# Optimization experiments

Hardware: AMD Instinct MI355X
Metric: run time of the kernel (lower is better)

The kernel has to match this reference:

```python
import jax, jax.numpy as jnp
import numpy as np

DIM = 96
HEADS = 6
WS = 8                      # window_size
OWS = int(WS * 0.5) + WS    # overlap_win_size = 12
PAD = (OWS - WS) // 2       # 2
Dd = Hh = Ww = 24
B = 1
L = Dd * Hh * Ww
MLP_H = DIM * 2
TBL = (WS + OWS - 1) ** 3   # 6859 relative-position-bias entries


def setup_inputs() -> dict:
    key = jax.random.key(0)
    ks = jax.random.split(key, 8)
    def n(k, shape, s=0.02):
        return jax.random.normal(k, shape, jnp.float32) * s
    return {
        "x": jax.random.normal(ks[0], (B, L, DIM), jnp.float32),
        "ln1_w": jnp.ones((DIM,), jnp.float32),
        "ln1_b": jnp.zeros((DIM,), jnp.float32),
        "qkv_w": n(ks[1], (3 * DIM, DIM)),
        "qkv_b": jnp.zeros((3 * DIM,), jnp.float32),
        "rpb": n(ks[2], (TBL, HEADS)),
        "proj_w": n(ks[3], (DIM, DIM)),
        "proj_b": jnp.zeros((DIM,), jnp.float32),
        "ln2_w": jnp.ones((DIM,), jnp.float32),
        "ln2_b": jnp.zeros((DIM,), jnp.float32),
        "fc1_w": n(ks[4], (MLP_H, DIM)),
        "fc1_b": jnp.zeros((MLP_H,), jnp.float32),
        "fc2_w": n(ks[5], (DIM, MLP_H)),
        "fc2_b": jnp.zeros((DIM,), jnp.float32),
        "rpi": jax.random.randint(ks[6], (WS ** 3, OWS ** 3), 0, TBL),
        "D": Dd, "H": Hh, "W": Ww,
    }


def _ln(x, w, b):
    m = jnp.mean(x, -1, keepdims=True)
    v = jnp.var(x, -1, keepdims=True)
    return (x - m) / jnp.sqrt(v + 1e-5) * w + b


def _ocab3d(x, ln1_w, ln1_b, qkv_w, qkv_b, rpb, proj_w, proj_b,
            ln2_w, ln2_b, fc1_w, fc1_b, fc2_w, fc2_b, rpi, D, H, W):
    Bz, Lz, C = x.shape
    hd = C // HEADS
    scale = hd ** -0.5
    shortcut = x

    xn = _ln(x, ln1_w, ln1_b).reshape(Bz, D, H, W, C)
    qkv = xn @ qkv_w.T + qkv_b                   # [B,D,H,W,3C]
    q = qkv[..., :C]
    kv = qkv[..., C:]                            # cat(k, v) on channels, [B,D,H,W,2C]

    nD, nH, nW = D // WS, H // WS, W // WS
    nw = nD * nH * nW

    # non-overlapping query windows -> [B*nw, WS^3, C]
    qw = q.reshape(Bz, nD, WS, nH, WS, nW, WS, C)
    qw = qw.transpose(0, 1, 3, 5, 2, 4, 6, 7).reshape(Bz * nw, WS ** 3, C)

    # overlapping kv windows via pad + strided gather (mirrors F.pad + unfold)
    kvp = jnp.pad(kv, ((0, 0), (PAD, PAD), (PAD, PAD), (PAD, PAD), (0, 0)))
    idx_d = (jnp.arange(nD) * WS)[:, None] + jnp.arange(OWS)[None, :]
    idx_h = (jnp.arange(nH) * WS)[:, None] + jnp.arange(OWS)[None, :]
    idx_w = (jnp.arange(nW) * WS)[:, None] + jnp.arange(OWS)[None, :]
    kw = kvp[:, idx_d]                 # [B,nD,OWS,Hp,Wp,2C]
    kw = kw[:, :, :, idx_h]            # [B,nD,OWS,nH,OWS,Wp,2C]
    kw = kw[:, :, :, :, :, idx_w]      # [B,nD,OWS,nH,OWS,nW,OWS,2C]
    kw = kw.transpose(0, 1, 3, 5, 2, 4, 6, 7).reshape(Bz * nw, OWS ** 3, 2 * C)
    kk, vv = kw[..., :C], kw[..., C:]

    qh = qw.reshape(-1, WS ** 3, HEADS, hd).transpose(0, 2, 1, 3) * scale
    kh = kk.reshape(-1, OWS ** 3, HEADS, hd).transpose(0, 2, 1, 3)
    vh = vv.reshape(-1, OWS ** 3, HEADS, hd).transpose(0, 2, 1, 3)

    attn = jnp.einsum('bhqd,bhkd->bhqk', qh, kh)               # [B*nw,H,512,1728]
    bias = rpb[rpi.reshape(-1)].reshape(WS ** 3, OWS ** 3, HEADS).transpose(2, 0, 1)
    attn = jax.nn.softmax(attn + bias[None], axis=-1)
    out = jnp.einsum('bhqk,bhkd->bhqd', attn, vh)
    out = out.transpose(0, 2, 1, 3).reshape(Bz * nw, WS ** 3, C)

    # window reverse -> [B, L, C]
    out = out.reshape(Bz, nD, nH, nW, WS, WS, WS, C)
    out = out.transpose(0, 1, 4, 2, 5, 3, 6, 7).reshape(Bz, D * H * W, C)

    x2 = out @ proj_w.T + proj_b + shortcut
    h1 = jax.nn.gelu(_ln(x2, ln2_w, ln2_b) @ fc1_w.T + fc1_b, approximate=False)
    return x2 + (h1 @ fc2_w.T + fc2_b)


def reference(x, ln1_w, ln1_b, qkv_w, qkv_b, rpb, proj_w, proj_b,
              ln2_w, ln2_b, fc1_w, fc1_b, fc2_w, fc2_b, rpi, D, H, W):
    return _ocab3d(x, ln1_w, ln1_b, qkv_w, qkv_b, rpb, proj_w, proj_b,
                   ln2_w, ln2_b, fc1_w, fc1_b, fc2_w, fc2_b, rpi, D, H, W)
```

## Files before the change

kernel.cpp:

```cpp
#include <hip/hip_runtime.h>
#include <math.h>

#define DIMC   96
#define NHEADS 6
#define HD     16
#define WSZ    8
#define OWSZ   12
#define PADW   2
#define DD     24
#define LTOK   13824
#define NWIN   27
#define NKEY   1728
#define NROW   512
#define MLPH   192
#define PDIM   28
#define PD3    21952
#define TBL    6859
#define LSTR   82944
#define AOSTR  1327104
#define LOG2E  1.4426950408889634f

typedef __attribute__((ext_vector_type(4))) short bf16x4;
typedef __attribute__((ext_vector_type(8))) short bf16x8;
typedef __attribute__((ext_vector_type(4))) float f32x4;

__device__ __forceinline__ unsigned short bfround(float f) {
    unsigned u = __float_as_uint(f);
    return (unsigned short)((u + 0x7FFFu + ((u >> 16) & 1u)) >> 16);
}
__device__ __forceinline__ unsigned bfpack(float a, float b) {
    unsigned ua = __float_as_uint(a), ub = __float_as_uint(b);
    ua = (ua + 0x7FFFu + ((ua >> 16) & 1u)) >> 16;
    ub = (ub + 0x7FFFu + ((ub >> 16) & 1u)) >> 16;
    return ua | (ub << 16);
}
__device__ __forceinline__ uint4 pack8(const float* v) {
    uint4 u;
    u.x = bfpack(v[0], v[1]); u.y = bfpack(v[2], v[3]);
    u.z = bfpack(v[4], v[5]); u.w = bfpack(v[6], v[7]);
    return u;
}
__device__ __forceinline__ bf16x4 pack4(f32x4 p) {
    union { uint2 u; bf16x4 v; } r;
    r.u.x = __builtin_amdgcn_perm(__float_as_uint(p[1]), __float_as_uint(p[0]), 0x07060302u);
    r.u.y = __builtin_amdgcn_perm(__float_as_uint(p[3]), __float_as_uint(p[2]), 0x07060302u);
    return r.v;
}
__device__ __forceinline__ f32x4 cvt4(uint2 b) {
    f32x4 c;
    c[0] = __uint_as_float(b.x << 16);
    c[1] = __uint_as_float(b.x & 0xffff0000u);
    c[2] = __uint_as_float(b.y << 16);
    c[3] = __uint_as_float(b.y & 0xffff0000u);
    return c;
}
__device__ __forceinline__ f32x4 mfma16(bf16x4 a, bf16x4 b, f32x4 c) {
#if __has_builtin(__builtin_amdgcn_mfma_f32_16x16x16bf16_1k)
    return __builtin_amdgcn_mfma_f32_16x16x16bf16_1k(a, b, c, 0, 0, 0);
#else
    bf16x8 a8 = {a[0], a[1], a[2], a[3], 0, 0, 0, 0};
    bf16x8 b8 = {b[0], b[1], b[2], b[3], 0, 0, 0, 0};
    return __builtin_amdgcn_mfma_f32_16x16x32_bf16(a8, b8, c, 0, 0, 0);
#endif
}
__device__ __forceinline__ f32x4 mfma32k(bf16x8 a, bf16x8 b, f32x4 c) {
    return __builtin_amdgcn_mfma_f32_16x16x32_bf16(a, b, c, 0, 0, 0);
}
__device__ __forceinline__ float fexp2(float x) {
#if __has_builtin(__builtin_amdgcn_exp2f)
    return __builtin_amdgcn_exp2f(x);
#else
    return exp2f(x);
#endif
}

#define QKVB 1296
#define ZB   515
#define WPB  45
#define BIASB 216
__global__ __launch_bounds__(256) void qkvz_kernel(
        const float* __restrict__ X, const float* __restrict__ W,
        const float* __restrict__ bias, const float* __restrict__ lnw,
        const float* __restrict__ lnb,
        const float* __restrict__ projw, const float* __restrict__ fc1w,
        const float* __restrict__ fc2w,
        const int* __restrict__ rpi, const float* __restrict__ rpb,
        unsigned short* __restrict__ q16, unsigned short* __restrict__ kvp2,
        uint4* __restrict__ wpack, unsigned short* __restrict__ biasP) {
    __shared__ uint4 Af4[2 * 3 * 4 * 16];
    __shared__ uint4 Bf4[6 * 3 * 4 * 16];
    int bx = blockIdx.x, tid = threadIdx.x;

    if (bx >= QKVB + ZB + WPB) {
        int b2 = bx - (QKVB + ZB + WPB);
        int c  = b2 % 27;
        int qp = b2 / 27;
        int quart = qp >> 1, qt = qp & 1;
        int quadp = (tid >> 4) & 3, m16p = tid & 15;
        int wavep = tid >> 6;
        int q = quart * 128 + wavep * 32 + qt * 16 + m16p;
        const int* rp = rpi + (long)q * NKEY + c * 64 + quadp * 8;
        uint2 h[6][4];
        #pragma unroll
        for (int kt = 0; kt < 4; ++kt) {
            int4 t = *(const int4*)(rp + (kt >> 1) * 32 + (kt & 1) * 4);
            const float* b0 = rpb + (long)t.x * 6;
            const float* b1 = rpb + (long)t.y * 6;
            const float* b2p = rpb + (long)t.z * 6;
            const float* b3 = rpb + (long)t.w * 6;
            float4 q0 = *(const float4*)b0; float2 r0 = *(const float2*)(b0 + 4);
            float4 q1 = *(const float4*)b1; float2 r1 = *(const float2*)(b1 + 4);
            float4 q2 = *(const float4*)b2p; float2 r2 = *(const float2*)(b2p + 4);
            float4 q3 = *(const float4*)b3; float2 r3 = *(const float2*)(b3 + 4);
            h[0][kt].x = bfpack(q0.x * LOG2E, q1.x * LOG2E);
            h[0][kt].y = bfpack(q2.x * LOG2E, q3.x * LOG2E);
            h[1][kt].x = bfpack(q0.y * LOG2E, q1.y * LOG2E);
            h[1][kt].y = bfpack(q2.y * LOG2E, q3.y * LOG2E);
            h[2][kt].x = bfpack(q0.z * LOG2E, q1.z * LOG2E);
            h[2][kt].y = bfpack(q2.z * LOG2E, q3.z * LOG2E);
            h[3][kt].x = bfpack(q0.w * LOG2E, q1.w * LOG2E);
            h[3][kt].y = bfpack(q2.w * LOG2E, q3.w * LOG2E);
            h[4][kt].x = bfpack(r0.x * LOG2E, r1.x * LOG2E);
            h[4][kt].y = bfpack(r2.x * LOG2E, r3.x * LOG2E);
            h[5][kt].x = bfpack(r0.y * LOG2E, r1.y * LOG2E);
            h[5][kt].y = bfpack(r2.y * LOG2E, r3.y * LOG2E);
        }
        long ob = qt * 4096 + tid * 16;
        #pragma unroll
        for (int head = 0; head < 6; ++head) {
            unsigned short* o = biasP + ((long)(head * 4 + quart) * 27 + c) * 8192 + ob;
            *(uint4*)(o)     = make_uint4(h[head][0].x, h[head][0].y,
                                          h[head][1].x, h[head][1].y);
            *(uint4*)(o + 8) = make_uint4(h[head][2].x, h[head][2].y,
                                          h[head][3].x, h[head][3].y);
        }
        return;
    }
    if (bx >= QKVB + ZB) {
        int u = (bx - QKVB - ZB) * 256 + tid;
        if (u < 5760) {
            int p = (u < 1152) ? u : (u < 3456 ? (u - 1152) % 1152 : (u - 3456) % 1152);
            int nn = p & 15, r = p >> 4, qg = r & 3, r2 = r >> 2;
            int kt = r2 % 3, ct = r2 / 3;
            int n = ct * 16 + nn, g = kt * 4 + qg;
            const float* src;
            if (u < 1152)      src = projw + n * 96 + g * 8;
            else if (u < 3456) { int nc = (u - 1152) / 1152; src = fc1w + (long)(nc * 96 + n) * 96 + g * 8; }
            else               { int kh = (u - 3456) / 1152; src = fc2w + (long)n * 192 + kh * 96 + g * 8; }
            const float4* s4 = (const float4*)src;
            float v[8];
            float4 t0 = s4[0], t1 = s4[1];
            v[0]=t0.x; v[1]=t0.y; v[2]=t0.z; v[3]=t0.w;
            v[4]=t1.x; v[5]=t1.y; v[6]=t1.z; v[7]=t1.w;
            wpack[u] = pack8(v);
        }
        return;
    }
    if (bx >= QKVB) {
        int t = (bx - QKVB) * 256 + tid;
        if (t < 21952 * 6) {
            int head = t / PD3, pos = t % PD3;
            int d = pos / 784, h = (pos / 28) % 28, w = pos % 28;
            if (d < 2 || d >= 26 || h < 2 || h >= 26 || w < 2 || w >= 26) {
                uint4* p = (uint4*)(kvp2 + ((long)head * PD3 + pos) * 32);
                uint4 z = make_uint4(0, 0, 0, 0);
                p[0] = z; p[1] = z; p[2] = z; p[3] = z;
            }
        }
        return;
    }

    int nc   = bx % 3;
    int row0 = (bx / 3) * 32;

    if (tid < 128) {
        int row = tid >> 2, part = tid & 3;
        int rt = row >> 4, mm = row & 15;
        float v[24];
        const float4* xp = (const float4*)(X + (long)(row0 + row) * 96 + part * 24);
        float s = 0.f, sq = 0.f;
        #pragma unroll
        for (int i = 0; i < 6; ++i) {
            float4 t = xp[i];
            v[i*4+0] = t.x; v[i*4+1] = t.y; v[i*4+2] = t.z; v[i*4+3] = t.w;
            s  += t.x + t.y + t.z + t.w;
            sq += t.x*t.x + t.y*t.y + t.z*t.z + t.w*t.w;
        }
        s  += __shfl_xor(s, 1);  s  += __shfl_xor(s, 2);
        sq += __shfl_xor(sq, 1); sq += __shfl_xor(sq, 2);
        float mean = s * (1.f / 96.f);
        float inv  = rsqrtf(sq * (1.f / 96.f) - mean * mean + 1e-5f);
        const float4* wp = (const float4*)(lnw + part * 24);
        const float4* bp = (const float4*)(lnb + part * 24);
        #pragma unroll
        for (int i = 0; i < 6; ++i) {
            float4 wv = wp[i], bv = bp[i];
            v[i*4+0] = (v[i*4+0] - mean) * inv * wv.x + bv.x;
            v[i*4+1] = (v[i*4+1] - mean) * inv * wv.y + bv.y;
            v[i*4+2] = (v[i*4+2] - mean) * inv * wv.z + bv.z;
            v[i*4+3] = (v[i*4+3] - mean) * inv * wv.w + bv.w;
        }
        #pragma unroll
        for (int gg = 0; gg < 3; ++gg) {
            int g = part * 3 + gg;
            int kt = g >> 2, qq = g & 3;
            Af4[((rt * 3 + kt) * 4 + qq) * 16 + mm] = pack8(v + gg * 8);
        }
    }
    for (int idx = tid; idx < 96 * 12; idx += 256) {
        int n = idx / 12;
        int g = idx % 12;
        const float4* wp = (const float4*)(W + (long)(nc * 96 + n) * 96 + g * 8);
        float v[8];
        float4 t0 = wp[0], t1 = wp[1];
        v[0]=t0.x; v[1]=t0.y; v[2]=t0.z; v[3]=t0.w;
        v[4]=t1.x; v[5]=t1.y; v[6]=t1.z; v[7]=t1.w;
        int ct = n >> 4, nn = n & 15, kt = g >> 2, qg = g & 3;
        Bf4[((ct * 3 + kt) * 4 + qg) * 16 + nn] = pack8(v);
    }
    __syncthreads();

    int wave = tid >> 6, lane = tid & 63;
    int qq = lane >> 4, mI = lane & 15;
    int rt = wave & 1, cg = wave >> 1;

    f32x4 acc[3];
    #pragma unroll
    for (int j = 0; j < 3; ++j) acc[j] = (f32x4){0.f, 0.f, 0.f, 0.f};
    #pragma unroll
    for (int kt = 0; kt < 3; ++kt) {
        bf16x8 a = *(const bf16x8*)&Af4[((rt * 3 + kt) * 4 + qq) * 16 + mI];
        #pragma unroll
        for (int j = 0; j < 3; ++j) {
            bf16x8 b = *(const bf16x8*)&Bf4[(((cg * 3 + j) * 3 + kt) * 4 + qq) * 16 + mI];
            acc[j] = __builtin_amdgcn_mfma_f32_16x16x32_bf16(a, b, acc[j], 0, 0, 0);
        }
    }

    float bv[3];
    #pragma unroll
    for (int j = 0; j < 3; ++j) bv[j] = bias[nc * 96 + (cg * 3 + j) * 16 + mI];
    #pragma unroll
    for (int r = 0; r < 4; ++r) {
        int row = row0 + rt * 16 + qq * 4 + r;
        if (nc == 0) {
            unsigned short* op = q16 + (long)row * 96;
            #pragma unroll
            for (int j = 0; j < 3; ++j)
                op[(cg * 3 + j) * 16 + mI] = bfround(0.25f * LOG2E * (acc[j][r] + bv[j]));
        } else {
            int d = row / 576, hh = (row / 24) % 24, w2 = row % 24;
            long pos = ((long)(d + 2) * 28 + (hh + 2)) * 28 + (w2 + 2);
            #pragma unroll
            for (int j = 0; j < 3; ++j) {
                int head = cg * 3 + j;
                kvp2[((long)head * PD3 + pos) * 32 +
                     (nc == 2 ? 16 : 0) + mI] = bfround(acc[j][r] + bv[j]);
            }
        }
    }
}

#define KSTR 20
#define VKP  66

#define ATTN_STEP(P, BCUR, BNXT)                                              \
    {                                                                         \
        bool more = (cc + (P) + 1 < cn);                                      \
        if (more) stgn = *kvaddr(c0 + cc + (P) + 1);                          \
        __syncthreads();                                                      \
        bf16x4 kf[4];                                                         \
        _Pragma("unroll")                                                     \
        for (int kt = 0; kt < 4; ++kt)                                        \
            kf[kt] = *(const bf16x4*)&Ks[(P)][(kt * 16 + m16) * KSTR + quad * 4]; \
        bf16x8 vb0 = *(const bf16x8*)&Vt[(P)][m16 * VKP + quad * 8];          \
        bf16x8 vb1 = *(const bf16x8*)&Vt[(P)][m16 * VKP + 32 + quad * 8];     \
        f32x4 S[2][4];                                                        \
        _Pragma("unroll")                                                     \
        for (int qt = 0; qt < 2; ++qt) {                                      \
            _Pragma("unroll")                                                 \
            for (int kt = 0; kt < 4; ++kt) {                                  \
                uint4 bj = BCUR[qt][kt >> 1];                                 \
                uint2 bb = (kt & 1) ? make_uint2(bj.z, bj.w)                  \
                                    : make_uint2(bj.x, bj.y);                 \
                S[qt][kt] = mfma16(kf[kt], qf[qt], cvt4(bb));                 \
            }                                                                 \
        }                                                                     \
        if (more) {                                                           \
            const unsigned short* bp = bbase + (long)(c0 + cc + (P) + 1) * 8192 \
                                       + tid * 16;                            \
            _Pragma("unroll")                                                 \
            for (int qt = 0; qt < 2; ++qt) {                                  \
                BNXT[qt][0] = *(const uint4*)(bp + qt * 4096);                \
                BNXT[qt][1] = *(const uint4*)(bp + qt * 4096 + 8);            \
            }                                                                 \
        }                                                                     \
        bf16x8 P8[2][2];                                                      \
        _Pragma("unroll")                                                     \
        for (int qt = 0; qt < 2; ++qt) {                                      \
            _Pragma("unroll")                                                 \
            for (int u = 0; u < 2; ++u) {                                     \
                f32x4 p0, p1;                                                 \
                _Pragma("unroll")                                             \
                for (int r = 0; r < 4; ++r) {                                 \
                    p0[r] = fexp2(S[qt][2 * u][r]);                           \
                    p1[r] = fexp2(S[qt][2 * u + 1][r]);                       \
                }                                                             \
                union { struct { bf16x4 lo, hi; } h; bf16x8 v; } uu;          \
                uu.h.lo = pack4(p0); uu.h.hi = pack4(p1);                     \
                P8[qt][u] = uu.v;                                             \
                lacc[qt] = mfma32k(P8[qt][u], ones8, lacc[qt]);               \
            }                                                                 \
        }                                                                     \
        o[0] = mfma32k(P8[0][0], vb0, o[0]);                                  \
        o[1] = mfma32k(P8[1][0], vb0, o[1]);                                  \
        o[0] = mfma32k(P8[0][1], vb1, o[0]);                                  \
        o[1] = mfma32k(P8[1][1], vb1, o[1]);                                  \
        if (more) writeLDS((P) ^ 1, stgn);                                    \
    }

__global__ __launch_bounds__(256, 3) void attn_kernel(
        const unsigned short* __restrict__ q, const unsigned short* __restrict__ kvp2,
        const unsigned short* __restrict__ biasP, float* __restrict__ ao,
        float* __restrict__ lbuf) {
    __shared__ unsigned short Ks[2][64 * KSTR];
    __shared__ unsigned short Vt[2][16 * VKP];
    int bid = blockIdx.x;
    int w = bid / 48, rem = bid % 48;
    int head = rem >> 3;
    int quart = (rem >> 1) & 3, half = rem & 1;
    int wd8 = (w / 9) * 8, wh8 = ((w / 3) % 3) * 8, ww8 = (w % 3) * 8;
    int tid = threadIdx.x, wave = tid >> 6, lane = tid & 63;
    int quad = lane >> 4, m16 = lane & 15;
    int key = tid >> 2, part = tid & 3;
    int c0 = half ? 13 : 0;
    int cn = half ? 14 : 13;

    int skey = (key & 35) | ((key & 4) << 2) | ((key >> 1) & 12);

    auto kvaddr = [&](int c) -> const uint4* {
        int jg = c * 64 + key;
        int i = jg / 144, jh = (jg / 12) % 12, jw = jg % 12;
        long sp = ((long)(wd8 + i) * PDIM + (wh8 + jh)) * PDIM + (ww8 + jw);
        return (const uint4*)(kvp2 + ((long)head * PD3 + sp) * 32 + part * 8);
    };
    auto writeLDS = [&](int b, uint4 v) {
        if (part < 2) {
            *(uint2*)(&Ks[b][skey * KSTR + part * 8])     = make_uint2(v.x, v.y);
            *(uint2*)(&Ks[b][skey * KSTR + part * 8 + 4]) = make_uint2(v.z, v.w);
        } else {
            int d0 = (part - 2) * 8;
            unsigned short* vp = &Vt[b][d0 * VKP + key];
            vp[0 * VKP] = (unsigned short)(v.x);
            vp[1 * VKP] = (unsigned short)(v.x >> 16);
            vp[2 * VKP] = (unsigned short)(v.y);
            vp[3 * VKP] = (unsigned short)(v.y >> 16);
            vp[4 * VKP] = (unsigned short)(v.z);
            vp[5 * VKP] = (unsigned short)(v.z >> 16);
            vp[6 * VKP] = (unsigned short)(v.w);
            vp[7 * VKP] = (unsigned short)(v.w >> 16);
        }
    };

    bf16x4 qf[2];
    #pragma unroll
    for (int qt = 0; qt < 2; ++qt) {
        int ql = quart * 128 + wave * 32 + qt * 16 + m16;
        int ld = ql >> 6, lh = (ql >> 3) & 7, lw = ql & 7;
        int g = ((wd8 + ld) * 24 + (wh8 + lh)) * 24 + (ww8 + lw);
        qf[qt] = *(const bf16x4*)(q + (long)g * 96 + head * 16 + quad * 4);
    }

    const unsigned short* bbase = biasP + ((long)(head * 4 + quart) * 27) * 8192;
    uint4 bb0[2][2], bb1[2][2];
    {
        const unsigned short* bp = bbase + (long)c0 * 8192 + tid * 16;
        #pragma unroll
        for (int qt = 0; qt < 2; ++qt) {
            bb0[qt][0] = *(const uint4*)(bp + qt * 4096);
            bb0[qt][1] = *(const uint4*)(bp + qt * 4096 + 8);
        }
    }

    writeLDS(0, *kvaddr(c0));

    const bf16x8 ones8 = {(short)0x3F80, (short)0x3F80, (short)0x3F80, (short)0x3F80,
                          (short)0x3F80, (short)0x3F80, (short)0x3F80, (short)0x3F80};
    f32x4 o[2], lacc[2];
    o[0] = (f32x4){0.f,0.f,0.f,0.f}; o[1] = (f32x4){0.f,0.f,0.f,0.f};
    lacc[0] = o[0]; lacc[1] = o[1];
    uint4 stgn;

    for (int cc = 0; cc < cn; cc += 2) {
        ATTN_STEP(0, bb0, bb1)
        if (cc + 1 < cn) ATTN_STEP(1, bb1, bb0)
    }

    float* aout = ao + (long)half * AOSTR;
    float* lout = lbuf + (long)half * LSTR;
    #pragma unroll
    for (int qt = 0; qt < 2; ++qt) {
        #pragma unroll
        for (int r = 0; r < 4; ++r) {
            int ql = quart * 128 + wave * 32 + qt * 16 + quad * 4 + r;
            int ld = ql >> 6, lh = (ql >> 3) & 7, lw = ql & 7;
            int g = ((wd8 + ld) * 24 + (wh8 + lh)) * 24 + (ww8 + lw);
            aout[(long)g * 96 + head * 16 + m16] = o[qt][r];
            if (m16 == 0) lout[g * 6 + head] = lacc[qt][r];
        }
    }
}

#define X2S 100
__global__ __launch_bounds__(256) void mlp_kernel(
        const float* __restrict__ ao0, const float* __restrict__ ao1,
        const float* __restrict__ lbuf, const uint4* __restrict__ wpack,
        const float* __restrict__ projb, const float* __restrict__ x,
        const float* __restrict__ ln2w, const float* __restrict__ ln2b,
        const float* __restrict__ fc1b, const float* __restrict__ fc2b,
        float* __restrict__ out) {
    __shared__ uint4 Af4[2 * 3 * 4 * 16];
    __shared__ float x2s[32 * X2S];
    __shared__ unsigned short h16[32 * 192];
    int tid = threadIdx.x;
    int row0 = blockIdx.x * 32;
    int wave = tid >> 6, lane = tid & 63;
    int qq = lane >> 4, mI = lane & 15;
    int rt = wave & 1, cg = wave >> 1;

    if (tid < 128) {
        int row = tid >> 2, part = tid & 3;
        int rtA = row >> 4, mm = row & 15;
        int grow = row0 + row;
        const float4* a0 = (const float4*)(ao0 + (long)grow * 96 + part * 24);
        const float4* a1 = (const float4*)(ao1 + (long)grow * 96 + part * 24);
        int ha = (part * 3) >> 1, hb = ha + 1;
        float inva = 1.f / (lbuf[grow*6 + ha] + lbuf[LSTR + grow*6 + ha]);
        float invb = 1.f / (lbuf[grow*6 + hb] + lbuf[LSTR + grow*6 + hb]);
        float v[24];
        #pragma unroll
        for (int i = 0; i < 6; ++i) {
            float4 u0 = a0[i], u1 = a1[i];
            #pragma unroll
            for (int j = 0; j < 4; ++j) {
                int gc = part * 24 + i * 4 + j;
                float lv = ((gc >> 4) == ha) ? inva : invb;
                float s = (j==0?u0.x+u1.x : j==1?u0.y+u1.y : j==2?u0.z+u1.z : u0.w+u1.w);
                v[i*4+j] = s * lv;
            }
        }
        #pragma unroll
        for (int gg = 0; gg < 3; ++gg) {
            int g = part * 3 + gg;
            int kt = g >> 2, q4 = g & 3;
            Af4[((rtA * 3 + kt) * 4 + q4) * 16 + mm] = pack8(v + gg * 8);
        }
    }
    __syncthreads();

    {
        f32x4 acc[3];
        #pragma unroll
        for (int j = 0; j < 3; ++j) acc[j] = (f32x4){0.f,0.f,0.f,0.f};
        #pragma unroll
        for (int kt = 0; kt < 3; ++kt) {
            bf16x8 a = *(const bf16x8*)&Af4[((rt * 3 + kt) * 4 + qq) * 16 + mI];
            #pragma unroll
            for (int j = 0; j < 3; ++j) {
                bf16x8 b = *(const bf16x8*)&wpack[(((cg * 3 + j) * 3 + kt) * 4 + qq) * 16 + mI];
                acc[j] = __builtin_amdgcn_mfma_f32_16x16x32_bf16(a, b, acc[j], 0, 0, 0);
            }
        }
        float bv[3];
        #pragma unroll
        for (int j = 0; j < 3; ++j) bv[j] = projb[(cg * 3 + j) * 16 + mI];
        #pragma unroll
        for (int r = 0; r < 4; ++r) {
            int row = rt * 16 + qq * 4 + r;
            int grow = row0 + row;
            #pragma unroll
            for (int j = 0; j < 3; ++j) {
                int col = (cg * 3 + j) * 16 + mI;
                x2s[row * X2S + col] = acc[j][r] + bv[j] + x[(long)grow * 96 + col];
            }
        }
    }
    __syncthreads();

    if (tid < 128) {
        int row = tid >> 2, part = tid & 3;
        int rtA = row >> 4, mm = row & 15;
        float v[24];
        const float4* xp = (const float4*)(x2s + row * X2S + part * 24);
        float s = 0.f, sq = 0.f;
        #pragma unroll
        for (int i = 0; i < 6; ++i) {
            float4 t = xp[i];
            v[i*4+0] = t.x; v[i*4+1] = t.y; v[i*4+2] = t.z; v[i*4+3] = t.w;
            s  += t.x + t.y + t.z + t.w;
            sq += t.x*t.x + t.y*t.y + t.z*t.z + t.w*t.w;
        }
        s  += __shfl_xor(s, 1);  s  += __shfl_xor(s, 2);
        sq += __shfl_xor(sq, 1); sq += __shfl_xor(sq, 2);
        float mean = s * (1.f / 96.f);
        float inv  = rsqrtf(sq * (1.f / 96.f) - mean * mean + 1e-5f);
        const float4* wp = (const float4*)(ln2w + part * 24);
        const float4* bp = (const float4*)(ln2b + part * 24);
        #pragma unroll
        for (int i = 0; i < 6; ++i) {
            float4 wv = wp[i], bv = bp[i];
            v[i*4+0] = (v[i*4+0] - mean) * inv * wv.x + bv.x;
            v[i*4+1] = (v[i*4+1] - mean) * inv * wv.y + bv.y;
            v[i*4+2] = (v[i*4+2] - mean) * inv * wv.z + bv.z;
            v[i*4+3] = (v[i*4+3] - mean) * inv * wv.w + bv.w;
        }
        #pragma unroll
        for (int gg = 0; gg < 3; ++gg) {
            int g = part * 3 + gg;
            int kt = g >> 2, q4 = g & 3;
            Af4[((rtA * 3 + kt) * 4 + q4) * 16 + mm] = pack8(v + gg * 8);
        }
    }
    __syncthreads();

    #pragma unroll
    for (int nc = 0; nc < 2; ++nc) {
        f32x4 acc[3];
        #pragma unroll
        for (int j = 0; j < 3; ++j) acc[j] = (f32x4){0.f,0.f,0.f,0.f};
        #pragma unroll
        for (int kt = 0; kt < 3; ++kt) {
            bf16x8 a = *(const bf16x8*)&Af4[((rt * 3 + kt) * 4 + qq) * 16 + mI];
            #pragma unroll
            for (int j = 0; j < 3; ++j) {
                bf16x8 b = *(const bf16x8*)&wpack[1152 + nc * 1152 +
                               (((cg * 3 + j) * 3 + kt) * 4 + qq) * 16 + mI];
                acc[j] = __builtin_amdgcn_mfma_f32_16x16x32_bf16(a, b, acc[j], 0, 0, 0);
            }
        }
        float bv[3];
        #pragma unroll
        for (int j = 0; j < 3; ++j) bv[j] = fc1b[nc * 96 + (cg * 3 + j) * 16 + mI];
        #pragma unroll
        for (int r = 0; r < 4; ++r) {
            int row = rt * 16 + qq * 4 + r;
            #pragma unroll
            for (int j = 0; j < 3; ++j) {
                int col = nc * 96 + (cg * 3 + j) * 16 + mI;
                float v = acc[j][r] + bv[j];
                float g = 0.5f * v * (1.f + erff(v * 0.70710678f));
                int fi = (((row >> 4) * 6 + (col >> 5)) * 4 + ((col >> 3) & 3)) * 16 + (row & 15);
                h16[fi * 8 + (col & 7)] = bfround(g);
            }
        }
    }
    __syncthreads();

    f32x4 acc2[3];
    #pragma unroll
    for (int j = 0; j < 3; ++j) acc2[j] = (f32x4){0.f,0.f,0.f,0.f};
    #pragma unroll
    for (int kh = 0; kh < 2; ++kh) {
        #pragma unroll
        for (int kt = 0; kt < 3; ++kt) {
            int ktA = kh * 3 + kt;
            bf16x8 a = *(const bf16x8*)&h16[(((rt * 6 + ktA) * 4 + qq) * 16 + mI) * 8];
            #pragma unroll
            for (int j = 0; j < 3; ++j) {
                bf16x8 b = *(const bf16x8*)&wpack[3456 + kh * 1152 +
                               (((cg * 3 + j) * 3 + kt) * 4 + qq) * 16 + mI];
                acc2[j] = __builtin_amdgcn_mfma_f32_16x16x32_bf16(a, b, acc2[j], 0, 0, 0);
            }
        }
    }
    float bv[3];
    #pragma unroll
    for (int j = 0; j < 3; ++j) bv[j] = fc2b[(cg * 3 + j) * 16 + mI];
    #pragma unroll
    for (int r = 0; r < 4; ++r) {
        int row = rt * 16 + qq * 4 + r;
        int grow = row0 + row;
        #pragma unroll
        for (int j = 0; j < 3; ++j) {
            int col = (cg * 3 + j) * 16 + mI;
            out[(long)grow * 96 + col] = acc2[j][r] + bv[j] + x2s[row * X2S + col];
        }
    }
}

extern "C" void kernel_launch(void* const* d_in, const int* in_sizes, int n_in,
                              void* d_out, int out_size, void* d_ws, size_t ws_size,
                              hipStream_t stream) {
    const float* x     = (const float*)d_in[0];
    const float* ln1w  = (const float*)d_in[1];
    const float* ln1b  = (const float*)d_in[2];
    const float* qkvw  = (const float*)d_in[3];
    const float* qkvb  = (const float*)d_in[4];
    const float* rpb   = (const float*)d_in[5];
    const float* projw = (const float*)d_in[6];
    const float* projb = (const float*)d_in[7];
    const float* ln2w  = (const float*)d_in[8];
    const float* ln2b  = (const float*)d_in[9];
    const float* fc1w  = (const float*)d_in[10];
    const float* fc1b  = (const float*)d_in[11];
    const float* fc2w  = (const float*)d_in[12];
    const float* fc2b  = (const float*)d_in[13];
    const int*   rpi   = (const int*)d_in[14];
    float* outp = (float*)d_out;

    float* ws = (float*)d_ws;
    float*          aop    = ws;
    unsigned short* q16    = (unsigned short*)(ws + 2654208);
    unsigned short* kvp16  = (unsigned short*)(ws + 3317760);
    unsigned short* biasPh = (unsigned short*)(ws + 5425152);
    float*          lbuf   = ws + 10733568;
    uint4*          wpack  = (uint4*)(ws + 10899456);

    qkvz_kernel<<<QKVB + ZB + WPB + BIASB, 256, 0, stream>>>(
        x, qkvw, qkvb, ln1w, ln1b, projw, fc1w, fc2w, rpi, rpb,
        q16, kvp16, wpack, biasPh);
    attn_kernel<<<NWIN * NHEADS * 4 * 2, 256, 0, stream>>>(q16, kvp16, biasPh, aop, lbuf);
    mlp_kernel<<<LTOK / 32, 256, 0, stream>>>(aop, aop + AOSTR, lbuf, wpack, projb, x,
                                              ln2w, ln2b, fc1b, fc2b, outp);
}
```

Measured before the change: 161.4 us.

## Fuse QKV column blocks per row tile, deepen bias prefetch, stage MLP weights in LDS

Result: no change. 159.4 us (-1.2%).

```diff
diff --git a/kernel.cpp b/kernel.cpp
--- a/kernel.cpp
+++ b/kernel.cpp
@@ -74,7 +74,7 @@
 #endif
 }
 
-#define QKVB 1296
+#define QKVB 432
 #define ZB   515
 #define WPB  45
 #define BIASB 216
@@ -88,7 +88,7 @@
         unsigned short* __restrict__ q16, unsigned short* __restrict__ kvp2,
         uint4* __restrict__ wpack, unsigned short* __restrict__ biasP) {
     __shared__ uint4 Af4[2 * 3 * 4 * 16];
-    __shared__ uint4 Bf4[6 * 3 * 4 * 16];
+    __shared__ uint4 Bf4[3 * 1152];
     int bx = blockIdx.x, tid = threadIdx.x;
 
     if (bx >= QKVB + ZB + WPB) {
@@ -170,8 +170,7 @@
         return;
     }
 
-    int nc   = bx % 3;
-    int row0 = (bx / 3) * 32;
+    int row0 = bx * 32;
 
     if (tid < 128) {
         int row = tid >> 2, part = tid & 3;
@@ -207,16 +206,17 @@
             Af4[((rt * 3 + kt) * 4 + qq) * 16 + mm] = pack8(v + gg * 8);
         }
     }
-    for (int idx = tid; idx < 96 * 12; idx += 256) {
-        int n = idx / 12;
-        int g = idx % 12;
+    for (int idx = tid; idx < 3 * 1152; idx += 256) {
+        int nc = idx / 1152, p = idx % 1152;
+        int n = p / 12;
+        int g = p % 12;
         const float4* wp = (const float4*)(W + (long)(nc * 96 + n) * 96 + g * 8);
         float v[8];
         float4 t0 = wp[0], t1 = wp[1];
         v[0]=t0.x; v[1]=t0.y; v[2]=t0.z; v[3]=t0.w;
         v[4]=t1.x; v[5]=t1.y; v[6]=t1.z; v[7]=t1.w;
         int ct = n >> 4, nn = n & 15, kt = g >> 2, qg = g & 3;
-        Bf4[((ct * 3 + kt) * 4 + qg) * 16 + nn] = pack8(v);
+        Bf4[nc * 1152 + ((ct * 3 + kt) * 4 + qg) * 16 + nn] = pack8(v);
     }
     __syncthreads();
 
@@ -224,38 +224,45 @@
     int qq = lane >> 4, mI = lane & 15;
     int rt = wave & 1, cg = wave >> 1;
 
-    f32x4 acc[3];
-    #pragma unroll
-    for (int j = 0; j < 3; ++j) acc[j] = (f32x4){0.f, 0.f, 0.f, 0.f};
-    #pragma unroll
-    for (int kt = 0; kt < 3; ++kt) {
-        bf16x8 a = *(const bf16x8*)&Af4[((rt * 3 + kt) * 4 + qq) * 16 + mI];
-        #pragma unroll
-        for (int j = 0; j < 3; ++j) {
-            bf16x8 b = *(const bf16x8*)&Bf4[(((cg * 3 + j) * 3 + kt) * 4 + qq) * 16 + mI];
-            acc[j] = __builtin_amdgcn_mfma_f32_16x16x32_bf16(a, b, acc[j], 0, 0, 0);
-        }
-    }
-
-    float bv[3];
-    #pragma unroll
-    for (int j = 0; j < 3; ++j) bv[j] = bias[nc * 96 + (cg * 3 + j) * 16 + mI];
-    #pragma unroll
-    for (int r = 0; r < 4; ++r) {
-        int row = row0 + rt * 16 + qq * 4 + r;
-        if (nc == 0) {
-            unsigned short* op = q16 + (long)row * 96;
-            #pragma unroll
-            for (int j = 0; j < 3; ++j)
-                op[(cg * 3 + j) * 16 + mI] = bfround(0.25f * LOG2E * (acc[j][r] + bv[j]));
-        } else {
-            int d = row / 576, hh = (row / 24) % 24, w2 = row % 24;
-            long pos = ((long)(d + 2) * 28 + (hh + 2)) * 28 + (w2 + 2);
+    bf16x8 a[3];
+    #pragma unroll
+    for (int kt = 0; kt < 3; ++kt)
+        a[kt] = *(const bf16x8*)&Af4[((rt * 3 + kt) * 4 + qq) * 16 + mI];
+
+    #pragma unroll
+    for (int nc = 0; nc < 3; ++nc) {
+        f32x4 acc[3];
+        #pragma unroll
+        for (int j = 0; j < 3; ++j) acc[j] = (f32x4){0.f, 0.f, 0.f, 0.f};
+        #pragma unroll
+        for (int kt = 0; kt < 3; ++kt) {
             #pragma unroll
             for (int j = 0; j < 3; ++j) {
-                int head = cg * 3 + j;
-                kvp2[((long)head * PD3 + pos) * 32 +
-                     (nc == 2 ? 16 : 0) + mI] = bfround(acc[j][r] + bv[j]);
+                bf16x8 b = *(const bf16x8*)&Bf4[nc * 1152 +
+                               (((cg * 3 + j) * 3 + kt) * 4 + qq) * 16 + mI];
+                acc[j] = __builtin_amdgcn_mfma_f32_16x16x32_bf16(a[kt], b, acc[j], 0, 0, 0);
+            }
+        }
+        float bv[3];
+        #pragma unroll
+        for (int j = 0; j < 3; ++j) bv[j] = bias[nc * 96 + (cg * 3 + j) * 16 + mI];
+        #pragma unroll
+        for (int r = 0; r < 4; ++r) {
+            int row = row0 + rt * 16 + qq * 4 + r;
+            if (nc == 0) {
+                unsigned short* op = q16 + (long)row * 96;
+                #pragma unroll
+                for (int j = 0; j < 3; ++j)
+                    op[(cg * 3 + j) * 16 + mI] = bfround(0.25f * LOG2E * (acc[j][r] + bv[j]));
+            } else {
+                int d = row / 576, hh = (row / 24) % 24, w2 = row % 24;
+                long pos = ((long)(d + 2) * 28 + (hh + 2)) * 28 + (w2 + 2);
+                #pragma unroll
+                for (int j = 0; j < 3; ++j) {
+                    int head = cg * 3 + j;
+                    kvp2[((long)head * PD3 + pos) * 32 +
+                         (nc == 2 ? 16 : 0) + mI] = bfround(acc[j][r] + bv[j]);
+                }
             }
         }
     }
@@ -264,10 +271,10 @@
 #define KSTR 20
 #define VKP  66
 
-#define ATTN_STEP(P, BCUR, BNXT)                                              \
+#define ATTN_STEP(P, BB)                                                      \
     {                                                                         \
-        bool more = (cc + (P) + 1 < cn);                                      \
-        if (more) stgn = *kvaddr(c0 + cc + (P) + 1);                          \
+        bool morekv = (cc + (P) + 1 < cn);                                    \
+        if (morekv) stgn = *kvaddr(c0 + cc + (P) + 1);                        \
         __syncthreads();                                                      \
         bf16x4 kf[4];                                                         \
         _Pragma("unroll")                                                     \
@@ -280,19 +287,19 @@
         for (int qt = 0; qt < 2; ++qt) {                                      \
             _Pragma("unroll")                                                 \
             for (int kt = 0; kt < 4; ++kt) {                                  \
-                uint4 bj = BCUR[qt][kt >> 1];                                 \
+                uint4 bj = BB[qt][kt >> 1];                                   \
                 uint2 bb = (kt & 1) ? make_uint2(bj.z, bj.w)                  \
                                     : make_uint2(bj.x, bj.y);                 \
                 S[qt][kt] = mfma16(kf[kt], qf[qt], cvt4(bb));                 \
             }                                                                 \
         }                                                                     \
-        if (more) {                                                           \
-            const unsigned short* bp = bbase + (long)(c0 + cc + (P) + 1) * 8192 \
+        if (cc + (P) + 2 < cn) {                                              \
+            const unsigned short* bp = bbase + (long)(c0 + cc + (P) + 2) * 8192 \
                                        + tid * 16;                            \
             _Pragma("unroll")                                                 \
             for (int qt = 0; qt < 2; ++qt) {                                  \
-                BNXT[qt][0] = *(const uint4*)(bp + qt * 4096);                \
-                BNXT[qt][1] = *(const uint4*)(bp + qt * 4096 + 8);            \
+                BB[qt][0] = *(const uint4*)(bp + qt * 4096);                  \
+                BB[qt][1] = *(const uint4*)(bp + qt * 4096 + 8);              \
             }                                                                 \
         }                                                                     \
         bf16x8 P8[2][2];                                                      \
@@ -316,7 +323,7 @@
         o[1] = mfma32k(P8[1][0], vb0, o[1]);                                  \
         o[0] = mfma32k(P8[0][1], vb1, o[0]);                                  \
         o[1] = mfma32k(P8[1][1], vb1, o[1]);                                  \
-        if (more) writeLDS((P) ^ 1, stgn);                                    \
+        if (morekv) writeLDS((P) ^ 1, stgn);                                  \
     }
 
 __global__ __launch_bounds__(256, 3) void attn_kernel(
@@ -380,6 +387,12 @@
             bb0[qt][0] = *(const uint4*)(bp + qt * 4096);
             bb0[qt][1] = *(const uint4*)(bp + qt * 4096 + 8);
         }
+        const unsigned short* bp1 = bbase + (long)(c0 + 1) * 8192 + tid * 16;
+        #pragma unroll
+        for (int qt = 0; qt < 2; ++qt) {
+            bb1[qt][0] = *(const uint4*)(bp1 + qt * 4096);
+            bb1[qt][1] = *(const uint4*)(bp1 + qt * 4096 + 8);
+        }
     }
 
     writeLDS(0, *kvaddr(c0));
@@ -392,8 +405,8 @@
     uint4 stgn;
 
     for (int cc = 0; cc < cn; cc += 2) {
-        ATTN_STEP(0, bb0, bb1)
-        if (cc + 1 < cn) ATTN_STEP(1, bb1, bb0)
+        ATTN_STEP(0, bb0)
+        if (cc + 1 < cn) ATTN_STEP(1, bb1)
     }
 
     float* aout = ao + (long)half * AOSTR;
@@ -412,23 +425,26 @@
 }
 
 #define X2S 100
-__global__ __launch_bounds__(256) void mlp_kernel(
+__global__ __launch_bounds__(512) void mlp_kernel(
         const float* __restrict__ ao0, const float* __restrict__ ao1,
         const float* __restrict__ lbuf, const uint4* __restrict__ wpack,
         const float* __restrict__ projb, const float* __restrict__ x,
         const float* __restrict__ ln2w, const float* __restrict__ ln2b,
         const float* __restrict__ fc1b, const float* __restrict__ fc2b,
         float* __restrict__ out) {
-    __shared__ uint4 Af4[2 * 3 * 4 * 16];
-    __shared__ float x2s[32 * X2S];
-    __shared__ unsigned short h16[32 * 192];
+    __shared__ uint4 Ws[5760];
+    __shared__ uint4 Af4[4 * 3 * 4 * 16];
+    __shared__ float x2s[64 * X2S];
+    __shared__ unsigned short h16[64 * 192];
     int tid = threadIdx.x;
-    int row0 = blockIdx.x * 32;
+    int row0 = blockIdx.x * 64;
     int wave = tid >> 6, lane = tid & 63;
     int qq = lane >> 4, mI = lane & 15;
-    int rt = wave & 1, cg = wave >> 1;
-
-    if (tid < 128) {
+    int rt = wave & 3, cg = wave >> 2;
+
+    for (int idx = tid; idx < 5760; idx += 512) Ws[idx] = wpack[idx];
+
+    if (tid < 256) {
         int row = tid >> 2, part = tid & 3;
         int rtA = row >> 4, mm = row & 15;
         int grow = row0 + row;
@@ -467,7 +483,7 @@
             bf16x8 a = *(const bf16x8*)&Af4[((rt * 3 + kt) * 4 + qq) * 16 + mI];
             #pragma unroll
             for (int j = 0; j < 3; ++j) {
-                bf16x8 b = *(const bf16x8*)&wpack[(((cg * 3 + j) * 3 + kt) * 4 + qq) * 16 + mI];
+                bf16x8 b = *(const bf16x8*)&Ws[(((cg * 3 + j) * 3 + kt) * 4 + qq) * 16 + mI];
                 acc[j] = __builtin_amdgcn_mfma_f32_16x16x32_bf16(a, b, acc[j], 0, 0, 0);
             }
         }
@@ -487,7 +503,7 @@
     }
     __syncthreads();
 
-    if (tid < 128) {
+    if (tid < 256) {
         int row = tid >> 2, part = tid & 3;
         int rtA = row >> 4, mm = row & 15;
         float v[24];
@@ -533,7 +549,7 @@
             bf16x8 a = *(const bf16x8*)&Af4[((rt * 3 + kt) * 4 + qq) * 16 + mI];
             #pragma unroll
             for (int j = 0; j < 3; ++j) {
-                bf16x8 b = *(const bf16x8*)&wpack[1152 + nc * 1152 +
+                bf16x8 b = *(const bf16x8*)&Ws[1152 + nc * 1152 +
                                (((cg * 3 + j) * 3 + kt) * 4 + qq) * 16 + mI];
                 acc[j] = __builtin_amdgcn_mfma_f32_16x16x32_bf16(a, b, acc[j], 0, 0, 0);
             }
@@ -567,7 +583,7 @@
             bf16x8 a = *(const bf16x8*)&h16[(((rt * 6 + ktA) * 4 + qq) * 16 + mI) * 8];
             #pragma unroll
             for (int j = 0; j < 3; ++j) {
-                bf16x8 b = *(const bf16x8*)&wpack[3456 + kh * 1152 +
+                bf16x8 b = *(const bf16x8*)&Ws[3456 + kh * 1152 +
                                (((cg * 3 + j) * 3 + kt) * 4 + qq) * 16 + mI];
                 acc2[j] = __builtin_amdgcn_mfma_f32_16x16x32_bf16(a, b, acc2[j], 0, 0, 0);
             }
@@ -620,6 +636,6 @@
         x, qkvw, qkvb, ln1w, ln1b, projw, fc1w, fc2w, rpi, rpb,
         q16, kvp16, wpack, biasPh);
     attn_kernel<<<NWIN * NHEADS * 4 * 2, 256, 0, stream>>>(q16, kvp16, biasPh, aop, lbuf);
-    mlp_kernel<<<LTOK / 32, 256, 0, stream>>>(aop, aop + AOSTR, lbuf, wpack, projb, x,
+    mlp_kernel<<<LTOK / 64, 512, 0, stream>>>(aop, aop + AOSTR, lbuf, wpack, projb, x,
                                               ln2w, ln2b, fc1b, fc2b, outp);
 }
```
